# Kernel optimization log

Hardware: AMD Instinct MI355X
Metric: run time of the kernel (lower is better)

Reference implementation:

```python
import jax, jax.numpy as jnp
import numpy as np

D_MODEL = 1024
NUM_HEADS = 16
D_K = D_MODEL // NUM_HEADS


def setup_inputs() -> dict:
    key = jax.random.key(0)
    ks = jax.random.split(key, 11)
    B, T = 4, 2048
    s = 1.0 / np.sqrt(D_MODEL)
    inp = {
        "query": jax.random.normal(ks[0], (B, T, D_MODEL), jnp.float32),
        "key": jax.random.normal(ks[1], (B, T, D_MODEL), jnp.float32),
        "value": jax.random.normal(ks[2], (B, T, D_MODEL), jnp.float32),
        "Wq": jax.random.uniform(ks[3], (D_MODEL, D_MODEL), jnp.float32, -s, s),
        "bq": jax.random.uniform(ks[4], (D_MODEL,), jnp.float32, -s, s),
        "Wk": jax.random.uniform(ks[5], (D_MODEL, D_MODEL), jnp.float32, -s, s),
        "bk": jax.random.uniform(ks[6], (D_MODEL,), jnp.float32, -s, s),
        "Wv": jax.random.uniform(ks[7], (D_MODEL, D_MODEL), jnp.float32, -s, s),
        "bv": jax.random.uniform(ks[8], (D_MODEL,), jnp.float32, -s, s),
        "Wo": jax.random.uniform(ks[9], (D_MODEL, D_MODEL), jnp.float32, -s, s),
        "bo": jax.random.uniform(ks[10], (D_MODEL,), jnp.float32, -s, s),
    }
    return inp


def _split_heads(x):
    B, T, _ = x.shape
    return x.reshape(B, T, NUM_HEADS, D_K).transpose(0, 2, 1, 3)  # (B,H,T,dk)


def reference(query, key, value, Wq, bq, Wk, bk, Wv, bv, Wo, bo):
    q = _split_heads(query @ Wq + bq)   # (B,H,Tq,dk)
    k = _split_heads(key @ Wk + bk)     # (B,H,Tk,dk)
    v = _split_heads(value @ Wv + bv)   # (B,H,Tk,dk)
    scale = 1.0 / jnp.sqrt(jnp.asarray(D_K, q.dtype))
    scores = jnp.einsum("bhqd,bhkd->bhqk", q, k) * scale
    weights = jax.nn.softmax(scores, axis=-1)
    attn = jnp.einsum("bhqk,bhkd->bhqd", weights, v)  # (B,H,Tq,dk)
    B, H, T, dk = attn.shape
    attn = attn.transpose(0, 2, 1, 3).reshape(B, T, H * dk)
    return attn @ Wo + bo
```

## Files before the change

kernel.cpp:

```cpp
#include <hip/hip_runtime.h>
#include <hip/hip_bf16.h>
#include <stdint.h>


typedef __bf16 bf16x8 __attribute__((ext_vector_type(8)));
typedef short  v4s    __attribute__((ext_vector_type(4)));
typedef float  f32x4  __attribute__((ext_vector_type(4)));

#define LOG2E 1.44269504088896340736f

static __device__ __forceinline__ uint32_t f2bf(float x) {
  uint32_t u = __float_as_uint(x);
  u += 0x7fffu + ((u >> 16) & 1u);
  return u >> 16;
}
#if __has_builtin(__builtin_amdgcn_cvt_pk_bf16_f32)
static __device__ __forceinline__ uint32_t pk2bf(float a, float b) {
  typedef __bf16 b2 __attribute__((ext_vector_type(2)));
  union { b2 v; uint32_t u; } x;
  x.v = __builtin_amdgcn_cvt_pk_bf16_f32(a, b);
  return x.u;
}
#else
static __device__ __forceinline__ uint32_t pk2bf(float a, float b) {
  return f2bf(a) | (f2bf(b) << 16);
}
#endif
static __device__ __forceinline__ void gl2lds16(const void* g, void* l) {
  __builtin_amdgcn_global_load_lds(
      (const __attribute__((address_space(1))) uint32_t*)g,
      (__attribute__((address_space(3))) uint32_t*)l, 16, 0, 0);
}

__global__ void convert_inputs(const float* __restrict__ q, const float* __restrict__ k,
                               const float* __restrict__ v, uint16_t* __restrict__ qo,
                               uint16_t* __restrict__ ko, uint16_t* __restrict__ vo) {
  const float* src = blockIdx.y == 0 ? q : (blockIdx.y == 1 ? k : v);
  uint16_t*    dst = blockIdx.y == 0 ? qo : (blockIdx.y == 1 ? ko : vo);
  size_t idx = ((size_t)blockIdx.x * 256 + threadIdx.x) * 8;
  float4 a = *(const float4*)(src + idx);
  float4 b = *(const float4*)(src + idx + 4);
  uint4 o;
  o.x = pk2bf(a.x, a.y); o.y = pk2bf(a.z, a.w);
  o.z = pk2bf(b.x, b.y); o.w = pk2bf(b.z, b.w);
  *(uint4*)(dst + idx) = o;
}

__global__ void transpose_weights(const float* __restrict__ Wq, const float* __restrict__ Wk,
                                  const float* __restrict__ Wv, const float* __restrict__ Wo,
                                  uint16_t* __restrict__ out) {
  __shared__ float t[32][33];
  const float* W = blockIdx.z == 0 ? Wq : blockIdx.z == 1 ? Wk : blockIdx.z == 2 ? Wv : Wo;
  uint16_t* O = out + (size_t)blockIdx.z * 1048576;
  int tx = threadIdx.x & 31, ty = threadIdx.x >> 5;
  int r0 = blockIdx.y * 32, c0 = blockIdx.x * 32;
#pragma unroll
  for (int i = 0; i < 4; i++) t[ty + i * 8][tx] = W[(size_t)(r0 + ty + i * 8) * 1024 + c0 + tx];
  __syncthreads();
#pragma unroll
  for (int i = 0; i < 4; i++)
    O[(size_t)(c0 + ty + i * 8) * 1024 + r0 + tx] = (uint16_t)f2bf(t[tx][ty + i * 8]);
}

__global__ __launch_bounds__(256, 2)
void gemm_bt(const uint16_t* __restrict__ A, const uint16_t* __restrict__ Bt,
             const float* __restrict__ bias, void* __restrict__ Cout,
             int M, int N, int K, int mode, float oscale) {
  __shared__ uint16_t lA[128 * 64], lB[128 * 64];
  int tid = threadIdx.x, wave = tid >> 6, lane = tid & 63;
  int q = lane >> 4, c = lane & 15;
  int mBase = blockIdx.y * 128, nBase = blockIdx.x * 128;
  int wrow = wave & 1, wcol = wave >> 1;
  f32x4 acc[4][4] = {};

  int swz = ((lane & 7) ^ (lane >> 3)) * 8;
  const uint16_t* gA = A + (size_t)(mBase + wave * 32 + (lane >> 3)) * K + swz;
  const uint16_t* gB = Bt + (size_t)(nBase + wave * 32 + (lane >> 3)) * K + swz;
  int cs = c & 7;

  for (int kt = 0; kt < K / 64; kt++) {
    __syncthreads();
    int k0 = kt * 64;
#pragma unroll
    for (int it = 0; it < 4; it++) {
      gl2lds16(gA + (size_t)(it * 8) * K + k0, &lA[(wave * 32 + it * 8) * 64]);
      gl2lds16(gB + (size_t)(it * 8) * K + k0, &lB[(wave * 32 + it * 8) * 64]);
    }
    __syncthreads();
#pragma unroll
    for (int kk = 0; kk < 2; kk++) {
      bf16x8 af[4], bfr[4];
#pragma unroll
      for (int i = 0; i < 4; i++)
        af[i] = *(const bf16x8*)&lA[(wrow * 64 + i * 16 + c) * 64 + ((kk * 4 + q) ^ cs) * 8];
#pragma unroll
      for (int j = 0; j < 4; j++)
        bfr[j] = *(const bf16x8*)&lB[(wcol * 64 + j * 16 + c) * 64 + ((kk * 4 + q) ^ cs) * 8];
#pragma unroll
      for (int i = 0; i < 4; i++)
#pragma unroll
        for (int j = 0; j < 4; j++)
          acc[i][j] = __builtin_amdgcn_mfma_f32_16x16x32_bf16(af[i], bfr[j], acc[i][j], 0, 0, 0);
    }
  }

  float bb[4];
#pragma unroll
  for (int j = 0; j < 4; j++) bb[j] = bias[nBase + wcol * 64 + j * 16 + c];

  if (mode == 0) {
    float* Co = (float*)Cout;
#pragma unroll
    for (int i = 0; i < 4; i++)
#pragma unroll
      for (int j = 0; j < 4; j++) {
        int row = mBase + wrow * 64 + i * 16 + q * 4;
        int col = nBase + wcol * 64 + j * 16 + c;
#pragma unroll
        for (int r = 0; r < 4; r++) Co[(size_t)(row + r) * N + col] = acc[i][j][r] + bb[j];
      }
  } else if (mode == 1) {
    uint16_t* Co = (uint16_t*)Cout;
#pragma unroll
    for (int i = 0; i < 4; i++)
#pragma unroll
      for (int j = 0; j < 4; j++) {
        int row = mBase + wrow * 64 + i * 16 + q * 4;
        int col = nBase + wcol * 64 + j * 16 + c;
#pragma unroll
        for (int r = 0; r < 4; r++)
          Co[(size_t)(row + r) * N + col] = (uint16_t)f2bf((acc[i][j][r] + bb[j]) * oscale);
      }
  } else {
    uint16_t* Co = (uint16_t*)Cout;
#pragma unroll
    for (int i = 0; i < 4; i++)
#pragma unroll
      for (int j = 0; j < 4; j++) {
        int n = nBase + wcol * 64 + j * 16 + c;
        int h = n >> 6, d = n & 63;
        int m = mBase + wrow * 64 + i * 16 + q * 4;
        int b = m >> 11, t = m & 2047;
        uint32_t lo = pk2bf(acc[i][j][0] + bb[j], acc[i][j][1] + bb[j]);
        uint32_t hi = pk2bf(acc[i][j][2] + bb[j], acc[i][j][3] + bb[j]);
        *(uint2*)(Co + (size_t)((b * 16 + h) * 64 + d) * 2048 + t) = make_uint2(lo, hi);
      }
  }
}

__global__ __launch_bounds__(256, 2)
void attn(const uint16_t* __restrict__ Qp, const uint16_t* __restrict__ Kp,
          const uint16_t* __restrict__ Vt, uint16_t* __restrict__ Ob) {
  __shared__ uint16_t sK[128 * 64], sV[64 * 128];
  int tid = threadIdx.x, wave = tid >> 6, lane = tid & 63;
  int q = lane >> 4, c = lane & 15;
  int cs = c & 7;
  int bh = blockIdx.y, b = bh >> 4, h = bh & 15;
  int qbase = blockIdx.x * 128;
  int swz = ((lane & 7) ^ (lane >> 3)) * 8;

  {
    const uint16_t* gQ =
        Qp + (size_t)(b * 2048 + qbase + wave * 32 + (lane >> 3)) * 1024 + h * 64 + swz;
#pragma unroll
    for (int it = 0; it < 4; it++)
      gl2lds16(gQ + (size_t)(it * 8) * 1024, &sK[(wave * 32 + it * 8) * 64]);
  }
  __syncthreads();
  bf16x8 qf[2][2];
#pragma unroll
  for (int it = 0; it < 2; it++)
#pragma unroll
    for (int kk = 0; kk < 2; kk++)
      qf[it][kk] =
          *(const bf16x8*)&sK[(wave * 32 + it * 16 + c) * 64 + ((kk * 4 + q) ^ cs) * 8];

  f32x4 o[4][2] = {};
  float l[2] = {0.f, 0.f};

  const uint16_t* gK0 =
      Kp + (size_t)(b * 2048 + wave * 32 + (lane >> 3)) * 1024 + h * 64 + swz;
  const uint16_t* gV0 = Vt + (size_t)(bh * 64 + wave * 16 + q) * 2048;

  for (int kt = 0; kt < 16; kt++) {
    __syncthreads();
#pragma unroll
    for (int it = 0; it < 4; it++)
      gl2lds16(gK0 + (size_t)(kt * 128 + it * 8) * 1024, &sK[(wave * 32 + it * 8) * 64]);
#pragma unroll
    for (int it = 0; it < 4; it++) {
      int vch = (c ^ (((it & 1) * 4) | q)) * 8;
      gl2lds16(gV0 + (size_t)(it * 4) * 2048 + kt * 128 + vch,
               &sV[(wave * 16 + it * 4) * 128]);
    }
    __syncthreads();

    f32x4 s[8][2];
#pragma unroll
    for (int jt = 0; jt < 8; jt++) {
      bf16x8 a = *(const bf16x8*)&sK[(jt * 16 + c) * 64 + (q ^ cs) * 8];
#pragma unroll
      for (int it = 0; it < 2; it++)
        s[jt][it] = __builtin_amdgcn_mfma_f32_16x16x32_bf16(a, qf[it][0],
                                                            (f32x4){0.f, 0.f, 0.f, 0.f}, 0, 0, 0);
    }
#pragma unroll
    for (int jt = 0; jt < 8; jt++) {
      bf16x8 a = *(const bf16x8*)&sK[(jt * 16 + c) * 64 + ((4 + q) ^ cs) * 8];
#pragma unroll
      for (int it = 0; it < 2; it++)
        s[jt][it] = __builtin_amdgcn_mfma_f32_16x16x32_bf16(a, qf[it][1], s[jt][it], 0, 0, 0);
    }

    uint32_t pk[8][2][2];
#pragma unroll
    for (int it = 0; it < 2; it++) {
      float rs = 0.f;
#pragma unroll
      for (int jt = 0; jt < 8; jt++) {
        float p0 = __builtin_amdgcn_exp2f(s[jt][it][0]);
        float p1 = __builtin_amdgcn_exp2f(s[jt][it][1]);
        float p2 = __builtin_amdgcn_exp2f(s[jt][it][2]);
        float p3 = __builtin_amdgcn_exp2f(s[jt][it][3]);
        rs += (p0 + p1) + (p2 + p3);
        pk[jt][it][0] = pk2bf(p0, p1);
        pk[jt][it][1] = pk2bf(p2, p3);
      }
      rs += __shfl_xor(rs, 16);
      rs += __shfl_xor(rs, 32);
      l[it] += rs;
    }

#pragma unroll
    for (int ks = 0; ks < 8; ks++) {
#pragma unroll
      for (int mt = 0; mt < 4; mt++) {
        v4s a = *(const v4s*)&sV[(mt * 16 + c) * 128 + (((ks * 2 + (q >> 1)) ^ cs) * 8) +
                                 (q & 1) * 4];
#pragma unroll
        for (int it = 0; it < 2; it++) {
          union { uint32_t u[2]; v4s s4; } pb;
          pb.u[0] = pk[ks][it][0];
          pb.u[1] = pk[ks][it][1];
          o[mt][it] = __builtin_amdgcn_mfma_f32_16x16x16bf16_1k(a, pb.s4, o[mt][it], 0, 0, 0);
        }
      }
    }
  }

#pragma unroll
  for (int it = 0; it < 2; it++) {
    float inv = 1.0f / l[it];
    size_t trow = (size_t)(b * 2048 + qbase + wave * 32 + it * 16 + c) * 1024 + h * 64;
#pragma unroll
    for (int mt = 0; mt < 4; mt++) {
      uint32_t lo = pk2bf(o[mt][it][0] * inv, o[mt][it][1] * inv);
      uint32_t hi = pk2bf(o[mt][it][2] * inv, o[mt][it][3] * inv);
      *(uint2*)(Ob + trow + mt * 16 + q * 4) = make_uint2(lo, hi);
    }
  }
}

extern "C" void kernel_launch(void* const* d_in, const int* in_sizes, int n_in,
                              void* d_out, int out_size, void* d_ws, size_t ws_size,
                              hipStream_t stream) {
  (void)in_sizes; (void)n_in; (void)out_size; (void)ws_size;
  const float* query = (const float*)d_in[0];
  const float* key_  = (const float*)d_in[1];
  const float* value = (const float*)d_in[2];
  const float* Wq = (const float*)d_in[3]; const float* bq = (const float*)d_in[4];
  const float* Wk = (const float*)d_in[5]; const float* bk = (const float*)d_in[6];
  const float* Wv = (const float*)d_in[7]; const float* bv = (const float*)d_in[8];
  const float* Wo = (const float*)d_in[9]; const float* bo = (const float*)d_in[10];

  const size_t SZ = (size_t)8192 * 1024;
  uint16_t* buf0 = (uint16_t*)d_ws;
  uint16_t* buf1 = buf0 + SZ;
  uint16_t* buf2 = buf1 + SZ;
  uint16_t* buf3 = buf2 + SZ;
  uint16_t* wts  = buf3 + SZ;
  uint16_t* Wtq = wts;
  uint16_t* Wtk = wts + 1048576;
  uint16_t* Wtv = wts + 2097152;
  uint16_t* Wto = wts + 3145728;

  const float Cs = 0.125f * LOG2E;

  convert_inputs<<<dim3(4096, 3), 256, 0, stream>>>(query, key_, value, buf0, buf1, buf2);
  transpose_weights<<<dim3(32, 32, 4), 256, 0, stream>>>(Wq, Wk, Wv, Wo, wts);
  gemm_bt<<<dim3(8, 64), 256, 0, stream>>>(buf0, Wtq, bq, buf3, 8192, 1024, 1024, 1, Cs);
  gemm_bt<<<dim3(8, 64), 256, 0, stream>>>(buf1, Wtk, bk, buf0, 8192, 1024, 1024, 1, 1.0f);
  gemm_bt<<<dim3(8, 64), 256, 0, stream>>>(buf2, Wtv, bv, buf1, 8192, 1024, 1024, 2, 1.0f);
  attn<<<dim3(16, 64), 256, 0, stream>>>(buf3, buf0, buf1, buf2);
  gemm_bt<<<dim3(8, 64), 256, 0, stream>>>(buf2, Wto, bo, (float*)d_out, 8192, 1024, 1024, 0, 1.0f);
}
```

Before: 363.4 us.

## Double-buffer LDS in GEMM and attention, merge QKV projections into one launch

Both the GEMM body and the attention kernel now use two LDS buffers. The next K-tile (and V-tile) is issued into the spare buffer while MFMAs run on the current one, which cuts the loop down to one barrier per iteration. The three Q/K/V projection GEMMs become a single launch with blockIdx.z selecting the operands, and K/V outputs go to new workspace regions so the projections no longer overwrite their own inputs. This doubles LDS use per block (64KB), which may lower occupancy, and it needs a larger workspace.

```diff
diff --git a/kernel.cpp b/kernel.cpp
--- a/kernel.cpp
+++ b/kernel.cpp
@@ -62,14 +62,13 @@
     O[(size_t)(c0 + ty + i * 8) * 1024 + r0 + tx] = (uint16_t)f2bf(t[tx][ty + i * 8]);
 }
 
-__global__ __launch_bounds__(256, 2)
-void gemm_bt(const uint16_t* __restrict__ A, const uint16_t* __restrict__ Bt,
-             const float* __restrict__ bias, void* __restrict__ Cout,
-             int M, int N, int K, int mode, float oscale) {
-  __shared__ uint16_t lA[128 * 64], lB[128 * 64];
+static __device__ __forceinline__ void gemm_body(
+    const uint16_t* __restrict__ A, const uint16_t* __restrict__ Bt,
+    const float* __restrict__ bias, void* __restrict__ Cout,
+    int N, int K, int mode, float oscale, int mBase, int nBase,
+    uint16_t* __restrict__ lA, uint16_t* __restrict__ lB) {
   int tid = threadIdx.x, wave = tid >> 6, lane = tid & 63;
   int q = lane >> 4, c = lane & 15;
-  int mBase = blockIdx.y * 128, nBase = blockIdx.x * 128;
   int wrow = wave & 1, wcol = wave >> 1;
   f32x4 acc[4][4] = {};
 
@@ -77,31 +76,45 @@
   const uint16_t* gA = A + (size_t)(mBase + wave * 32 + (lane >> 3)) * K + swz;
   const uint16_t* gB = Bt + (size_t)(nBase + wave * 32 + (lane >> 3)) * K + swz;
   int cs = c & 7;
-
-  for (int kt = 0; kt < K / 64; kt++) {
-    __syncthreads();
-    int k0 = kt * 64;
-#pragma unroll
-    for (int it = 0; it < 4; it++) {
-      gl2lds16(gA + (size_t)(it * 8) * K + k0, &lA[(wave * 32 + it * 8) * 64]);
-      gl2lds16(gB + (size_t)(it * 8) * K + k0, &lB[(wave * 32 + it * 8) * 64]);
-    }
-    __syncthreads();
+  const int nkt = K / 64;
+
+#pragma unroll
+  for (int it = 0; it < 4; it++) {
+    gl2lds16(gA + (size_t)(it * 8) * K, &lA[(wave * 32 + it * 8) * 64]);
+    gl2lds16(gB + (size_t)(it * 8) * K, &lB[(wave * 32 + it * 8) * 64]);
+  }
+  __syncthreads();
+
+  int p = 0;
+  for (int kt = 0; kt < nkt; kt++) {
+    int pn = p ^ 1;
+    if (kt + 1 < nkt) {
+      int k0 = (kt + 1) * 64;
+#pragma unroll
+      for (int it = 0; it < 4; it++) {
+        gl2lds16(gA + (size_t)(it * 8) * K + k0, &lA[pn * 8192 + (wave * 32 + it * 8) * 64]);
+        gl2lds16(gB + (size_t)(it * 8) * K + k0, &lB[pn * 8192 + (wave * 32 + it * 8) * 64]);
+      }
+    }
+    const uint16_t* la = lA + p * 8192;
+    const uint16_t* lb = lB + p * 8192;
 #pragma unroll
     for (int kk = 0; kk < 2; kk++) {
       bf16x8 af[4], bfr[4];
 #pragma unroll
       for (int i = 0; i < 4; i++)
-        af[i] = *(const bf16x8*)&lA[(wrow * 64 + i * 16 + c) * 64 + ((kk * 4 + q) ^ cs) * 8];
+        af[i] = *(const bf16x8*)&la[(wrow * 64 + i * 16 + c) * 64 + ((kk * 4 + q) ^ cs) * 8];
 #pragma unroll
       for (int j = 0; j < 4; j++)
-        bfr[j] = *(const bf16x8*)&lB[(wcol * 64 + j * 16 + c) * 64 + ((kk * 4 + q) ^ cs) * 8];
+        bfr[j] = *(const bf16x8*)&lb[(wcol * 64 + j * 16 + c) * 64 + ((kk * 4 + q) ^ cs) * 8];
 #pragma unroll
       for (int i = 0; i < 4; i++)
 #pragma unroll
         for (int j = 0; j < 4; j++)
           acc[i][j] = __builtin_amdgcn_mfma_f32_16x16x32_bf16(af[i], bfr[j], acc[i][j], 0, 0, 0);
     }
+    __syncthreads();
+    p = pn;
   }
 
   float bb[4];
@@ -149,9 +162,34 @@
 }
 
 __global__ __launch_bounds__(256, 2)
+void gemm_qkv(const uint16_t* __restrict__ qb, const uint16_t* __restrict__ kb,
+              const uint16_t* __restrict__ vb, const uint16_t* __restrict__ Wtq,
+              const uint16_t* __restrict__ Wtk, const uint16_t* __restrict__ Wtv,
+              const float* __restrict__ bq, const float* __restrict__ bk,
+              const float* __restrict__ bv, uint16_t* __restrict__ Qp,
+              uint16_t* __restrict__ Kp, uint16_t* __restrict__ Vt, float cs) {
+  __shared__ uint16_t lA[2 * 8192], lB[2 * 8192];
+  int z = blockIdx.z;
+  const uint16_t* A  = z == 0 ? qb : (z == 1 ? kb : vb);
+  const uint16_t* Bt = z == 0 ? Wtq : (z == 1 ? Wtk : Wtv);
+  const float* bias  = z == 0 ? bq : (z == 1 ? bk : bv);
+  void* C            = z == 0 ? (void*)Qp : (z == 1 ? (void*)Kp : (void*)Vt);
+  int mode   = z == 2 ? 2 : 1;
+  float os   = z == 0 ? cs : 1.0f;
+  gemm_body(A, Bt, bias, C, 1024, 1024, mode, os, blockIdx.y * 128, blockIdx.x * 128, lA, lB);
+}
+
+__global__ __launch_bounds__(256, 2)
+void gemm_out(const uint16_t* __restrict__ A, const uint16_t* __restrict__ Bt,
+              const float* __restrict__ bias, float* __restrict__ C) {
+  __shared__ uint16_t lA[2 * 8192], lB[2 * 8192];
+  gemm_body(A, Bt, bias, C, 1024, 1024, 0, 1.0f, blockIdx.y * 128, blockIdx.x * 128, lA, lB);
+}
+
+__global__ __launch_bounds__(256, 2)
 void attn(const uint16_t* __restrict__ Qp, const uint16_t* __restrict__ Kp,
           const uint16_t* __restrict__ Vt, uint16_t* __restrict__ Ob) {
-  __shared__ uint16_t sK[128 * 64], sV[64 * 128];
+  __shared__ uint16_t sK[2][128 * 64], sV[2][64 * 128];
   int tid = threadIdx.x, wave = tid >> 6, lane = tid & 63;
   int q = lane >> 4, c = lane & 15;
   int cs = c & 7;
@@ -164,7 +202,7 @@
         Qp + (size_t)(b * 2048 + qbase + wave * 32 + (lane >> 3)) * 1024 + h * 64 + swz;
 #pragma unroll
     for (int it = 0; it < 4; it++)
-      gl2lds16(gQ + (size_t)(it * 8) * 1024, &sK[(wave * 32 + it * 8) * 64]);
+      gl2lds16(gQ + (size_t)(it * 8) * 1024, &sK[0][(wave * 32 + it * 8) * 64]);
   }
   __syncthreads();
   bf16x8 qf[2][2];
@@ -173,7 +211,8 @@
 #pragma unroll
     for (int kk = 0; kk < 2; kk++)
       qf[it][kk] =
-          *(const bf16x8*)&sK[(wave * 32 + it * 16 + c) * 64 + ((kk * 4 + q) ^ cs) * 8];
+          *(const bf16x8*)&sK[0][(wave * 32 + it * 16 + c) * 64 + ((kk * 4 + q) ^ cs) * 8];
+  __syncthreads();
 
   f32x4 o[4][2] = {};
   float l[2] = {0.f, 0.f};
@@ -182,23 +221,36 @@
       Kp + (size_t)(b * 2048 + wave * 32 + (lane >> 3)) * 1024 + h * 64 + swz;
   const uint16_t* gV0 = Vt + (size_t)(bh * 64 + wave * 16 + q) * 2048;
 
+#pragma unroll
+  for (int it = 0; it < 4; it++)
+    gl2lds16(gK0 + (size_t)(it * 8) * 1024, &sK[0][(wave * 32 + it * 8) * 64]);
+#pragma unroll
+  for (int it = 0; it < 4; it++) {
+    int vch = (c ^ (((it & 1) * 4) | q)) * 8;
+    gl2lds16(gV0 + (size_t)(it * 4) * 2048 + vch, &sV[0][(wave * 16 + it * 4) * 128]);
+  }
+  __syncthreads();
+
+  int p = 0;
   for (int kt = 0; kt < 16; kt++) {
-    __syncthreads();
-#pragma unroll
-    for (int it = 0; it < 4; it++)
-      gl2lds16(gK0 + (size_t)(kt * 128 + it * 8) * 1024, &sK[(wave * 32 + it * 8) * 64]);
-#pragma unroll
-    for (int it = 0; it < 4; it++) {
-      int vch = (c ^ (((it & 1) * 4) | q)) * 8;
-      gl2lds16(gV0 + (size_t)(it * 4) * 2048 + kt * 128 + vch,
-               &sV[(wave * 16 + it * 4) * 128]);
-    }
-    __syncthreads();
+    int pn = p ^ 1;
+    if (kt + 1 < 16) {
+#pragma unroll
+      for (int it = 0; it < 4; it++)
+        gl2lds16(gK0 + (size_t)((kt + 1) * 128 + it * 8) * 1024,
+                 &sK[pn][(wave * 32 + it * 8) * 64]);
+#pragma unroll
+      for (int it = 0; it < 4; it++) {
+        int vch = (c ^ (((it & 1) * 4) | q)) * 8;
+        gl2lds16(gV0 + (size_t)(it * 4) * 2048 + (kt + 1) * 128 + vch,
+                 &sV[pn][(wave * 16 + it * 4) * 128]);
+      }
+    }
 
     f32x4 s[8][2];
 #pragma unroll
     for (int jt = 0; jt < 8; jt++) {
-      bf16x8 a = *(const bf16x8*)&sK[(jt * 16 + c) * 64 + (q ^ cs) * 8];
+      bf16x8 a = *(const bf16x8*)&sK[p][(jt * 16 + c) * 64 + (q ^ cs) * 8];
 #pragma unroll
       for (int it = 0; it < 2; it++)
         s[jt][it] = __builtin_amdgcn_mfma_f32_16x16x32_bf16(a, qf[it][0],
@@ -206,7 +258,7 @@
     }
 #pragma unroll
     for (int jt = 0; jt < 8; jt++) {
-      bf16x8 a = *(const bf16x8*)&sK[(jt * 16 + c) * 64 + ((4 + q) ^ cs) * 8];
+      bf16x8 a = *(const bf16x8*)&sK[p][(jt * 16 + c) * 64 + ((4 + q) ^ cs) * 8];
 #pragma unroll
       for (int it = 0; it < 2; it++)
         s[jt][it] = __builtin_amdgcn_mfma_f32_16x16x32_bf16(a, qf[it][1], s[jt][it], 0, 0, 0);
@@ -235,8 +287,8 @@
     for (int ks = 0; ks < 8; ks++) {
 #pragma unroll
       for (int mt = 0; mt < 4; mt++) {
-        v4s a = *(const v4s*)&sV[(mt * 16 + c) * 128 + (((ks * 2 + (q >> 1)) ^ cs) * 8) +
-                                 (q & 1) * 4];
+        v4s a = *(const v4s*)&sV[p][(mt * 16 + c) * 128 + (((ks * 2 + (q >> 1)) ^ cs) * 8) +
+                                    (q & 1) * 4];
 #pragma unroll
         for (int it = 0; it < 2; it++) {
           union { uint32_t u[2]; v4s s4; } pb;
@@ -246,6 +298,8 @@
         }
       }
     }
+    __syncthreads();
+    p = pn;
   }
 
 #pragma unroll
@@ -288,9 +342,12 @@
 
   convert_inputs<<<dim3(4096, 3), 256, 0, stream>>>(query, key_, value, buf0, buf1, buf2);
   transpose_weights<<<dim3(32, 32, 4), 256, 0, stream>>>(Wq, Wk, Wv, Wo, wts);
-  gemm_bt<<<dim3(8, 64), 256, 0, stream>>>(buf0, Wtq, bq, buf3, 8192, 1024, 1024, 1, Cs);
-  gemm_bt<<<dim3(8, 64), 256, 0, stream>>>(buf1, Wtk, bk, buf0, 8192, 1024, 1024, 1, 1.0f);
-  gemm_bt<<<dim3(8, 64), 256, 0, stream>>>(buf2, Wtv, bv, buf1, 8192, 1024, 1024, 2, 1.0f);
-  attn<<<dim3(16, 64), 256, 0, stream>>>(buf3, buf0, buf1, buf2);
-  gemm_bt<<<dim3(8, 64), 256, 0, stream>>>(buf2, Wto, bo, (float*)d_out, 8192, 1024, 1024, 0, 1.0f);
-}
+  gemm_qkv<<<dim3(8, 64, 3), 256, 0, stream>>>(buf0, buf1, buf2, Wtq, Wtk, Wtv,
+                                               bq, bk, bv,
+                                               buf3,
+                                               wts + 4194304,
+                                               wts + 4194304 + SZ,
+                                               Cs);
+  attn<<<dim3(16, 64), 256, 0, stream>>>(buf3, wts + 4194304, wts + 4194304 + SZ, buf2);
+  gemm_out<<<dim3(8, 64), 256, 0, stream>>>(buf2, Wto, bo, (float*)d_out);
+}
```

After: 362.5 us. No clear change (-0.2%).

## Merge QKV projections into one launch and interleave QK/PV in attention

Applied to the files above, without the earlier changes.

The three Q/K/V projection GEMMs now run as one grid-z batched launch. This removes launch gaps and the tail imbalance of small grids, and it needs separate workspace buffers for Kp and Vt so the inputs are not overwritten. The attention inner loop now computes scores, exp2 and PV accumulation per 16-key tile instead of materialising all 8 score tiles first. That lowers register pressure and lets the MFMA and exp work interleave. The row-sum shuffle reduction is also deferred to the end of the loop instead of running every iteration.

```diff
diff --git a/kernel.cpp b/kernel.cpp
--- a/kernel.cpp
+++ b/kernel.cpp
@@ -62,14 +62,13 @@
     O[(size_t)(c0 + ty + i * 8) * 1024 + r0 + tx] = (uint16_t)f2bf(t[tx][ty + i * 8]);
 }
 
-__global__ __launch_bounds__(256, 2)
-void gemm_bt(const uint16_t* __restrict__ A, const uint16_t* __restrict__ Bt,
-             const float* __restrict__ bias, void* __restrict__ Cout,
-             int M, int N, int K, int mode, float oscale) {
-  __shared__ uint16_t lA[128 * 64], lB[128 * 64];
+static __device__ __forceinline__ void gemm_body(
+    const uint16_t* __restrict__ A, const uint16_t* __restrict__ Bt,
+    const float* __restrict__ bias, void* __restrict__ Cout,
+    int N, int K, int mode, float oscale, int mBase, int nBase,
+    uint16_t* __restrict__ lA, uint16_t* __restrict__ lB) {
   int tid = threadIdx.x, wave = tid >> 6, lane = tid & 63;
   int q = lane >> 4, c = lane & 15;
-  int mBase = blockIdx.y * 128, nBase = blockIdx.x * 128;
   int wrow = wave & 1, wcol = wave >> 1;
   f32x4 acc[4][4] = {};
 
@@ -146,6 +145,31 @@
         *(uint2*)(Co + (size_t)((b * 16 + h) * 64 + d) * 2048 + t) = make_uint2(lo, hi);
       }
   }
+}
+
+__global__ __launch_bounds__(256, 2)
+void gemm_qkv(const uint16_t* __restrict__ qb, const uint16_t* __restrict__ kb,
+              const uint16_t* __restrict__ vb, const uint16_t* __restrict__ Wtq,
+              const uint16_t* __restrict__ Wtk, const uint16_t* __restrict__ Wtv,
+              const float* __restrict__ bq, const float* __restrict__ bk,
+              const float* __restrict__ bv, uint16_t* __restrict__ Qp,
+              uint16_t* __restrict__ Kp, uint16_t* __restrict__ Vt, float cs) {
+  __shared__ uint16_t lA[8192], lB[8192];
+  int z = blockIdx.z;
+  const uint16_t* A  = z == 0 ? qb : (z == 1 ? kb : vb);
+  const uint16_t* Bt = z == 0 ? Wtq : (z == 1 ? Wtk : Wtv);
+  const float* bias  = z == 0 ? bq : (z == 1 ? bk : bv);
+  void* C            = z == 0 ? (void*)Qp : (z == 1 ? (void*)Kp : (void*)Vt);
+  int mode   = z == 2 ? 2 : 1;
+  float os   = z == 0 ? cs : 1.0f;
+  gemm_body(A, Bt, bias, C, 1024, 1024, mode, os, blockIdx.y * 128, blockIdx.x * 128, lA, lB);
+}
+
+__global__ __launch_bounds__(256, 2)
+void gemm_out(const uint16_t* __restrict__ A, const uint16_t* __restrict__ Bt,
+              const float* __restrict__ bias, float* __restrict__ C) {
+  __shared__ uint16_t lA[8192], lB[8192];
+  gemm_body(A, Bt, bias, C, 1024, 1024, 0, 1.0f, blockIdx.y * 128, blockIdx.x * 128, lA, lB);
 }
 
 __global__ __launch_bounds__(256, 2)
@@ -176,7 +200,7 @@
           *(const bf16x8*)&sK[(wave * 32 + it * 16 + c) * 64 + ((kk * 4 + q) ^ cs) * 8];
 
   f32x4 o[4][2] = {};
-  float l[2] = {0.f, 0.f};
+  float rs0 = 0.f, rs1 = 0.f;
 
   const uint16_t* gK0 =
       Kp + (size_t)(b * 2048 + wave * 32 + (lane >> 3)) * 1024 + h * 64 + swz;
@@ -195,58 +219,40 @@
     }
     __syncthreads();
 
-    f32x4 s[8][2];
 #pragma unroll
     for (int jt = 0; jt < 8; jt++) {
-      bf16x8 a = *(const bf16x8*)&sK[(jt * 16 + c) * 64 + (q ^ cs) * 8];
-#pragma unroll
-      for (int it = 0; it < 2; it++)
-        s[jt][it] = __builtin_amdgcn_mfma_f32_16x16x32_bf16(a, qf[it][0],
-                                                            (f32x4){0.f, 0.f, 0.f, 0.f}, 0, 0, 0);
-    }
-#pragma unroll
-    for (int jt = 0; jt < 8; jt++) {
-      bf16x8 a = *(const bf16x8*)&sK[(jt * 16 + c) * 64 + ((4 + q) ^ cs) * 8];
-#pragma unroll
-      for (int it = 0; it < 2; it++)
-        s[jt][it] = __builtin_amdgcn_mfma_f32_16x16x32_bf16(a, qf[it][1], s[jt][it], 0, 0, 0);
-    }
-
-    uint32_t pk[8][2][2];
-#pragma unroll
-    for (int it = 0; it < 2; it++) {
-      float rs = 0.f;
-#pragma unroll
-      for (int jt = 0; jt < 8; jt++) {
-        float p0 = __builtin_amdgcn_exp2f(s[jt][it][0]);
-        float p1 = __builtin_amdgcn_exp2f(s[jt][it][1]);
-        float p2 = __builtin_amdgcn_exp2f(s[jt][it][2]);
-        float p3 = __builtin_amdgcn_exp2f(s[jt][it][3]);
-        rs += (p0 + p1) + (p2 + p3);
-        pk[jt][it][0] = pk2bf(p0, p1);
-        pk[jt][it][1] = pk2bf(p2, p3);
+      bf16x8 a0 = *(const bf16x8*)&sK[(jt * 16 + c) * 64 + (q ^ cs) * 8];
+      bf16x8 a1 = *(const bf16x8*)&sK[(jt * 16 + c) * 64 + ((4 + q) ^ cs) * 8];
+      f32x4 s0 = __builtin_amdgcn_mfma_f32_16x16x32_bf16(a0, qf[0][0],
+                                                         (f32x4){0.f, 0.f, 0.f, 0.f}, 0, 0, 0);
+      s0 = __builtin_amdgcn_mfma_f32_16x16x32_bf16(a1, qf[0][1], s0, 0, 0, 0);
+      f32x4 s1 = __builtin_amdgcn_mfma_f32_16x16x32_bf16(a0, qf[1][0],
+                                                         (f32x4){0.f, 0.f, 0.f, 0.f}, 0, 0, 0);
+      s1 = __builtin_amdgcn_mfma_f32_16x16x32_bf16(a1, qf[1][1], s1, 0, 0, 0);
+
+      float p00 = __builtin_amdgcn_exp2f(s0[0]), p01 = __builtin_amdgcn_exp2f(s0[1]);
+      float p02 = __builtin_amdgcn_exp2f(s0[2]), p03 = __builtin_amdgcn_exp2f(s0[3]);
+      float p10 = __builtin_amdgcn_exp2f(s1[0]), p11 = __builtin_amdgcn_exp2f(s1[1]);
+      float p12 = __builtin_amdgcn_exp2f(s1[2]), p13 = __builtin_amdgcn_exp2f(s1[3]);
+      rs0 += (p00 + p01) + (p02 + p03);
+      rs1 += (p10 + p11) + (p12 + p13);
+      union { uint32_t u[2]; v4s s4; } pb0, pb1;
+      pb0.u[0] = pk2bf(p00, p01); pb0.u[1] = pk2bf(p02, p03);
+      pb1.u[0] = pk2bf(p10, p11); pb1.u[1] = pk2bf(p12, p13);
+
+#pragma unroll
+      for (int mt = 0; mt < 4; mt++) {
+        v4s a = *(const v4s*)&sV[(mt * 16 + c) * 128 + (((jt * 2 + (q >> 1)) ^ cs) * 8) +
+                                 (q & 1) * 4];
+        o[mt][0] = __builtin_amdgcn_mfma_f32_16x16x16bf16_1k(a, pb0.s4, o[mt][0], 0, 0, 0);
+        o[mt][1] = __builtin_amdgcn_mfma_f32_16x16x16bf16_1k(a, pb1.s4, o[mt][1], 0, 0, 0);
       }
-      rs += __shfl_xor(rs, 16);
-      rs += __shfl_xor(rs, 32);
-      l[it] += rs;
-    }
-
-#pragma unroll
-    for (int ks = 0; ks < 8; ks++) {
-#pragma unroll
-      for (int mt = 0; mt < 4; mt++) {
-        v4s a = *(const v4s*)&sV[(mt * 16 + c) * 128 + (((ks * 2 + (q >> 1)) ^ cs) * 8) +
-                                 (q & 1) * 4];
-#pragma unroll
-        for (int it = 0; it < 2; it++) {
-          union { uint32_t u[2]; v4s s4; } pb;
-          pb.u[0] = pk[ks][it][0];
-          pb.u[1] = pk[ks][it][1];
-          o[mt][it] = __builtin_amdgcn_mfma_f32_16x16x16bf16_1k(a, pb.s4, o[mt][it], 0, 0, 0);
-        }
-      }
-    }
-  }
+    }
+  }
+
+  rs0 += __shfl_xor(rs0, 16); rs0 += __shfl_xor(rs0, 32);
+  rs1 += __shfl_xor(rs1, 16); rs1 += __shfl_xor(rs1, 32);
+  float l[2] = {rs0, rs1};
 
 #pragma unroll
   for (int it = 0; it < 2; it++) {
@@ -283,14 +289,15 @@
   uint16_t* Wtk = wts + 1048576;
   uint16_t* Wtv = wts + 2097152;
   uint16_t* Wto = wts + 3145728;
+  uint16_t* Kp  = wts + 4194304;
+  uint16_t* Vt  = Kp + SZ;
 
   const float Cs = 0.125f * LOG2E;
 
   convert_inputs<<<dim3(4096, 3), 256, 0, stream>>>(query, key_, value, buf0, buf1, buf2);
   transpose_weights<<<dim3(32, 32, 4), 256, 0, stream>>>(Wq, Wk, Wv, Wo, wts);
-  gemm_bt<<<dim3(8, 64), 256, 0, stream>>>(buf0, Wtq, bq, buf3, 8192, 1024, 1024, 1, Cs);
-  gemm_bt<<<dim3(8, 64), 256, 0, stream>>>(buf1, Wtk, bk, buf0, 8192, 1024, 1024, 1, 1.0f);
-  gemm_bt<<<dim3(8, 64), 256, 0, stream>>>(buf2, Wtv, bv, buf1, 8192, 1024, 1024, 2, 1.0f);
-  attn<<<dim3(16, 64), 256, 0, stream>>>(buf3, buf0, buf1, buf2);
-  gemm_bt<<<dim3(8, 64), 256, 0, stream>>>(buf2, Wto, bo, (float*)d_out, 8192, 1024, 1024, 0, 1.0f);
-}
+  gemm_qkv<<<dim3(8, 64, 3), 256, 0, stream>>>(buf0, buf1, buf2, Wtq, Wtk, Wtv,
+                                               bq, bk, bv, buf3, Kp, Vt, Cs);
+  attn<<<dim3(16, 64), 256, 0, stream>>>(buf3, Kp, Vt, buf2);
+  gemm_out<<<dim3(8, 64), 256, 0, stream>>>(buf2, Wto, bo, (float*)d_out);
+}
```

Measured after the change: 355.3 us. -2.2%, faster.
